# Kernel optimization log

Measured on AMD Instinct MI355X. Metric: run time of the kernel, lower is better.

The kernel has to match this reference:

```python
import jax, jax.numpy as jnp
import numpy as np

N_NODES = 50000
N_EDGES = 800000
D_IN = 128
D_OUT = 128


def _seg_mean(values, seg_ids, num_segments):
    # values: [E, D] gathered messages; seg_ids: [E] destination ids
    s = jax.ops.segment_sum(values, seg_ids, num_segments=num_segments)
    deg = jax.ops.segment_sum(jnp.ones((values.shape[0],), values.dtype), seg_ids,
                              num_segments=num_segments)
    # DGL mean aggregation yields 0 for zero in-degree nodes
    return jnp.where(deg[:, None] > 0, s / jnp.maximum(deg, 1.0)[:, None], 0.0)


def setup_inputs() -> dict:
    key = jax.random.key(0)
    k1, k2, k3, k4, k5 = jax.random.split(key, 5)
    feat = jax.random.normal(k1, (N_NODES, D_IN), dtype=jnp.float32)
    src = jax.random.randint(k2, (N_EDGES,), 0, N_NODES, dtype=jnp.int32)
    dst = jax.random.randint(k3, (N_EDGES,), 0, N_NODES, dtype=jnp.int32)
    W = jax.random.normal(k4, (D_OUT, 3 * D_IN), dtype=jnp.float32) * (1.0 / np.sqrt(3 * D_IN))
    b = jax.random.normal(k5, (D_OUT,), dtype=jnp.float32) * 0.01
    return {"feat": feat, "src": src, "dst": dst, "W": W, "b": b}


def reference(feat, src, dst, W, b):
    n = feat.shape[0]
    # forward direction: message from src -> dst, mean over in-neighbors
    fwd_neigh = _seg_mean(feat[src], dst, n)          # [N, D]
    # backward direction: graph.reverse() swaps src/dst
    bwd_neigh = _seg_mean(feat[dst], src, n)          # [N, D]
    h = jnp.concatenate((feat, fwd_neigh, bwd_neigh), axis=1)  # [N, 3D]
    return h @ W.T + b
```

## Files before the change

kernel.cpp:

```cpp
#include <hip/hip_runtime.h>

#define DIM 128
#define CAP 64
#define CHUNK 2048

typedef __attribute__((ext_vector_type(8))) short bf16x8;
typedef __attribute__((ext_vector_type(4))) float f32x4;
typedef __attribute__((ext_vector_type(2))) float f32x2;

__device__ __forceinline__ unsigned short f2b(float f) {
  unsigned int u = __float_as_uint(f);
  return (unsigned short)((u + 0x7FFFu + ((u >> 16) & 1u)) >> 16);
}
__device__ __forceinline__ float blo(unsigned int v) { return __uint_as_float(v << 16); }
__device__ __forceinline__ float bhi(unsigned int v) { return __uint_as_float(v & 0xFFFF0000u); }

__global__ __launch_bounds__(256) void k_bin(const int* __restrict__ src,
                                             const int* __restrict__ dst,
                                             unsigned int* __restrict__ scrF,
                                             unsigned int* __restrict__ scrB,
                                             int* __restrict__ offsF,
                                             int* __restrict__ offsB, int E) {
  __shared__ int fc[256], bc[256], fo[256], bo[256], sa[256], sb2[256];
  __shared__ unsigned int linf[CHUNK], linb[CHUNK];
  const int t = threadIdx.x;
  const int base = blockIdx.x * CHUNK;
  const int n = min(CHUNK, E - base);
  fc[t] = 0; bc[t] = 0;
  __syncthreads();
  int fbk[8], fsl[8], bsl[8], bbk[8];
  unsigned int fvv[8], bvv[8];
  #pragma unroll
  for (int j = 0; j < 8; ++j) {
    int e = base + j * 256 + t;
    fbk[j] = -1;
    if (e < E) {
      int s = src[e], d = dst[e];
      fbk[j] = d >> 8; fvv[j] = ((unsigned int)(d & 255) << 16) | (unsigned int)s;
      bbk[j] = s >> 8; bvv[j] = ((unsigned int)(s & 255) << 16) | (unsigned int)d;
      fsl[j] = atomicAdd(&fc[fbk[j]], 1);
      bsl[j] = atomicAdd(&bc[bbk[j]], 1);
    }
  }
  __syncthreads();
  sa[t] = fc[t]; sb2[t] = bc[t];
  __syncthreads();
  #pragma unroll
  for (int s = 1; s < 256; s <<= 1) {
    int va = sa[t] + ((t >= s) ? sa[t - s] : 0);
    int vb = sb2[t] + ((t >= s) ? sb2[t - s] : 0);
    __syncthreads();
    sa[t] = va; sb2[t] = vb;
    __syncthreads();
  }
  fo[t] = sa[t] - fc[t];
  bo[t] = sb2[t] - bc[t];
  __syncthreads();
  #pragma unroll
  for (int j = 0; j < 8; ++j) {
    if (fbk[j] >= 0) {
      linf[fo[fbk[j]] + fsl[j]] = fvv[j];
      linb[bo[bbk[j]] + bsl[j]] = bvv[j];
    }
  }
  offsF[blockIdx.x * 256 + t] = fo[t];
  offsB[blockIdx.x * 256 + t] = bo[t];
  __syncthreads();
  for (int k = t; k < n; k += 256) {
    scrF[base + k] = linf[k];
    scrB[base + k] = linb[k];
  }
}

__global__ __launch_bounds__(512) void k_gemmcsr(
    const float* __restrict__ feat, const float* __restrict__ W,
    const float* __restrict__ bias,
    unsigned short* __restrict__ g1b, unsigned char* __restrict__ g2f8,
    unsigned char* __restrict__ g3f8,
    const unsigned int* __restrict__ scrF, const unsigned int* __restrict__ scrB,
    const int* __restrict__ offsF, const int* __restrict__ offsB,
    unsigned short* __restrict__ fnbr, unsigned short* __restrict__ bnbr,
    int* __restrict__ degF, int* __restrict__ degB,
    int N, int E, int nblk, int nbkt, int G) {
  __shared__ __align__(16) unsigned char smem[98304];
  const int t = threadIdx.x;

  if ((int)blockIdx.x < 2 * nbkt) {
    int* ncnt = (int*)smem;
    unsigned short* nbuf = (unsigned short*)(smem + 1024);
    const int b = blockIdx.x >> 1;
    const int dir = blockIdx.x & 1;
    const unsigned int* scr = dir ? scrB : scrF;
    const int* offs = dir ? offsB : offsF;
    if (t < 256) ncnt[t] = 0;
    __syncthreads();
    for (int i = t; i < nblk; i += 512) {
      int o = offs[i * 256 + b];
      int n = min(CHUNK, E - i * CHUNK);
      int nxt = (b < 255) ? offs[i * 256 + b + 1] : n;
      int cb = i * CHUNK;
      for (int k = o; k < nxt; ++k) {
        unsigned int v = scr[cb + k];
        int node8 = v >> 16;
        int slot = atomicAdd(&ncnt[node8], 1);
        if (slot < CAP) nbuf[node8 * CAP + slot] = (unsigned short)(v & 0xFFFFu);
      }
    }
    __syncthreads();
    const int node0 = b * 256;
    const int nvalid = min(256, N - node0);
    if (nvalid <= 0) return;
    unsigned short* outp = (dir ? bnbr : fnbr) + (size_t)node0 * CAP;
    for (int idx = t; idx < nvalid * CAP; idx += 512)
      outp[idx] = nbuf[idx];
    int* deg = dir ? degB : degF;
    for (int u = t; u < nvalid; u += 512) deg[node0 + u] = ncnt[u];
    return;
  }

  for (int i = t; i < 12288; i += 512) {
    int flat = i * 4;
    int o = flat / 384;
    int kk = flat - o * 384;
    int n = (kk >> 7) * 128 + o;
    int k0 = kk & 127;
    float4 v = *(const float4*)(W + flat);
    ushort4 u; u.x = f2b(v.x); u.y = f2b(v.y); u.z = f2b(v.z); u.w = f2b(v.w);
    *(ushort4*)(smem + ((n * 256 + k0 * 2) ^ ((n & 7) << 4))) = u;
  }
  __syncthreads();

  const int wave = t >> 6, lane = t & 63;
  const int lr = lane & 15, lk = lane >> 4;
  float bv[8];
  #pragma unroll
  for (int i = 0; i < 8; ++i) bv[i] = bias[i * 16 + lr];

  const int MT = (N + 31) >> 5;
  const int TW = G * 8;
  for (int mt = (blockIdx.x - 2 * nbkt) * 8 + wave; mt < MT; mt += TW) {
    const int m0 = mt * 32;
    const bool two = (m0 + 16 < N);
    bf16x8 a0[4], a1[4];
    #pragma unroll
    for (int kc = 0; kc < 4; ++kc) {
      const float* p = feat + (size_t)(m0 + lr) * DIM + kc * 32 + lk * 8;
      float4 u = *(const float4*)p;
      float4 w = *(const float4*)(p + 4);
      bf16x8 r;
      r[0] = f2b(u.x); r[1] = f2b(u.y); r[2] = f2b(u.z); r[3] = f2b(u.w);
      r[4] = f2b(w.x); r[5] = f2b(w.y); r[6] = f2b(w.z); r[7] = f2b(w.w);
      a0[kc] = r;
    }
    if (two) {
      #pragma unroll
      for (int kc = 0; kc < 4; ++kc) {
        const float* p = feat + (size_t)(m0 + 16 + lr) * DIM + kc * 32 + lk * 8;
        float4 u = *(const float4*)p;
        float4 w = *(const float4*)(p + 4);
        bf16x8 r;
        r[0] = f2b(u.x); r[1] = f2b(u.y); r[2] = f2b(u.z); r[3] = f2b(u.w);
        r[4] = f2b(w.x); r[5] = f2b(w.y); r[6] = f2b(w.z); r[7] = f2b(w.w);
        a1[kc] = r;
      }
    }
    #pragma unroll
    for (int nf = 0; nf < 24; ++nf) {
      f32x4 acc0 = (f32x4){0.f, 0.f, 0.f, 0.f};
      f32x4 acc1 = (f32x4){0.f, 0.f, 0.f, 0.f};
      const int n = nf * 16 + lr;
      #pragma unroll
      for (int kc = 0; kc < 4; ++kc) {
        bf16x8 bw = *(const bf16x8*)(smem +
            ((n * 256 + kc * 64 + lk * 16) ^ ((n & 7) << 4)));
        acc0 = __builtin_amdgcn_mfma_f32_16x16x32_bf16(a0[kc], bw, acc0, 0, 0, 0);
        if (two)
          acc1 = __builtin_amdgcn_mfma_f32_16x16x32_bf16(a1[kc], bw, acc1, 0, 0, 0);
      }
      const int sec = nf >> 3;
      const int c0 = (nf & 7) * 16 + lr;
      if (sec == 0) {
        #pragma unroll
        for (int j = 0; j < 4; ++j) {
          g1b[(size_t)(m0 + lk * 4 + j) * DIM + c0] = f2b(acc0[j] + bv[nf & 7]);
          if (two)
            g1b[(size_t)(m0 + 16 + lk * 4 + j) * DIM + c0] = f2b(acc1[j] + bv[nf & 7]);
        }
      } else {
        unsigned char* gp = (sec == 1) ? g2f8 : g3f8;
        #pragma unroll
        for (int j = 0; j < 4; ++j) {
          unsigned int p8 = __builtin_amdgcn_cvt_pk_fp8_f32(acc0[j], acc0[j], 0, 0);
          gp[(size_t)(m0 + lk * 4 + j) * DIM + c0] = (unsigned char)p8;
          if (two) {
            unsigned int q8 = __builtin_amdgcn_cvt_pk_fp8_f32(acc1[j], acc1[j], 0, 0);
            gp[(size_t)(m0 + 16 + lk * 4 + j) * DIM + c0] = (unsigned char)q8;
          }
        }
      }
    }
  }
}

__global__ void k_aggregate(const unsigned char* __restrict__ g2f8,
                            const unsigned char* __restrict__ g3f8,
                            const unsigned short* __restrict__ g1b,
                            const int* __restrict__ degF, const int* __restrict__ degB,
                            const unsigned short* __restrict__ fnbr,
                            const unsigned short* __restrict__ bnbr,
                            float* __restrict__ out, int N) {
  int node = blockIdx.x * (blockDim.x >> 6) + (threadIdx.x >> 6);
  if (node >= N) return;
  const int lane = threadIdx.x & 63;
  const int qg = lane >> 4;
  const int sub = lane & 15;

  const int degf = degF[node], degb = degB[node];
  const int capf = min(degf, CAP), capb = min(degb, CAP);
  const int fid = fnbr[node * CAP + lane];
  const int bid = bnbr[node * CAP + lane];

  const uint2* gf = (const uint2*)g2f8;
  const uint2* gb = (const uint2*)g3f8;
  f32x2 f01 = {0.f, 0.f}, f23 = {0.f, 0.f}, f45 = {0.f, 0.f}, f67 = {0.f, 0.f};
  f32x2 b01 = {0.f, 0.f}, b23 = {0.f, 0.f}, b45 = {0.f, 0.f}, b67 = {0.f, 0.f};
  const int gmax = (max(capf, capb) + 3) >> 2;
  #pragma unroll 4
  for (int g = 0; g < gmax; ++g) {
    int k = 4 * g + qg;
    int rf = __shfl(fid, k);
    int rb = __shfl(bid, k);
    if (k < capf) {
      uint2 v = gf[rf * 16 + sub];
      f01 += __builtin_amdgcn_cvt_pk_f32_fp8(v.x, 0);
      f23 += __builtin_amdgcn_cvt_pk_f32_fp8(v.x, 1);
      f45 += __builtin_amdgcn_cvt_pk_f32_fp8(v.y, 0);
      f67 += __builtin_amdgcn_cvt_pk_f32_fp8(v.y, 1);
    }
    if (k < capb) {
      uint2 v = gb[rb * 16 + sub];
      b01 += __builtin_amdgcn_cvt_pk_f32_fp8(v.x, 0);
      b23 += __builtin_amdgcn_cvt_pk_f32_fp8(v.x, 1);
      b45 += __builtin_amdgcn_cvt_pk_f32_fp8(v.y, 0);
      b67 += __builtin_amdgcn_cvt_pk_f32_fp8(v.y, 1);
    }
  }
  float fa0 = f01[0], fa1 = f01[1], fa2 = f23[0], fa3 = f23[1];
  float fa4 = f45[0], fa5 = f45[1], fa6 = f67[0], fa7 = f67[1];
  float ba0 = b01[0], ba1 = b01[1], ba2 = b23[0], ba3 = b23[1];
  float ba4 = b45[0], ba5 = b45[1], ba6 = b67[0], ba7 = b67[1];
  fa0 += __shfl_xor(fa0, 16); fa0 += __shfl_xor(fa0, 32);
  fa1 += __shfl_xor(fa1, 16); fa1 += __shfl_xor(fa1, 32);
  fa2 += __shfl_xor(fa2, 16); fa2 += __shfl_xor(fa2, 32);
  fa3 += __shfl_xor(fa3, 16); fa3 += __shfl_xor(fa3, 32);
  fa4 += __shfl_xor(fa4, 16); fa4 += __shfl_xor(fa4, 32);
  fa5 += __shfl_xor(fa5, 16); fa5 += __shfl_xor(fa5, 32);
  fa6 += __shfl_xor(fa6, 16); fa6 += __shfl_xor(fa6, 32);
  fa7 += __shfl_xor(fa7, 16); fa7 += __shfl_xor(fa7, 32);
  ba0 += __shfl_xor(ba0, 16); ba0 += __shfl_xor(ba0, 32);
  ba1 += __shfl_xor(ba1, 16); ba1 += __shfl_xor(ba1, 32);
  ba2 += __shfl_xor(ba2, 16); ba2 += __shfl_xor(ba2, 32);
  ba3 += __shfl_xor(ba3, 16); ba3 += __shfl_xor(ba3, 32);
  ba4 += __shfl_xor(ba4, 16); ba4 += __shfl_xor(ba4, 32);
  ba5 += __shfl_xor(ba5, 16); ba5 += __shfl_xor(ba5, 32);
  ba6 += __shfl_xor(ba6, 16); ba6 += __shfl_xor(ba6, 32);
  ba7 += __shfl_xor(ba7, 16); ba7 += __shfl_xor(ba7, 32);

  if (lane < 16) {
    const float sf = (degf > 0) ? 1.0f / (float)degf : 0.0f;
    const float sb = (degb > 0) ? 1.0f / (float)degb : 0.0f;
    uint4 g1v = ((const uint4*)g1b)[node * 16 + lane];
    float4 u, v;
    u.x = blo(g1v.x) + fa0 * sf + ba0 * sb;
    u.y = bhi(g1v.x) + fa1 * sf + ba1 * sb;
    u.z = blo(g1v.y) + fa2 * sf + ba2 * sb;
    u.w = bhi(g1v.y) + fa3 * sf + ba3 * sb;
    v.x = blo(g1v.z) + fa4 * sf + ba4 * sb;
    v.y = bhi(g1v.z) + fa5 * sf + ba5 * sb;
    v.z = blo(g1v.w) + fa6 * sf + ba6 * sb;
    v.w = bhi(g1v.w) + fa7 * sf + ba7 * sb;
    float* op = out + node * DIM + lane * 8;
    *(float4*)op = u; *(float4*)(op + 4) = v;
  }
}

extern "C" void kernel_launch(void* const* d_in, const int* in_sizes, int n_in,
                              void* d_out, int out_size, void* d_ws, size_t ws_size,
                              hipStream_t stream) {
  (void)n_in; (void)out_size; (void)ws_size;
  const float* feat = (const float*)d_in[0];
  const int*   src  = (const int*)d_in[1];
  const int*   dst  = (const int*)d_in[2];
  const float* W    = (const float*)d_in[3];
  const float* bias = (const float*)d_in[4];
  float* out = (float*)d_out;
  const int N = in_sizes[0] / DIM;
  const int E = in_sizes[1];
  const int nblk = (E + CHUNK - 1) / CHUNK;
  const int nbkt = (N + 255) / 256;
  const int G = 192;

  char* ws = (char*)d_ws;
  size_t off = 0;
  auto take = [&](size_t bytes) -> void* {
    off = (off + 255) & ~(size_t)255;
    void* p = ws + off;
    off += bytes;
    return p;
  };
  unsigned int* scrF = (unsigned int*)take((size_t)nblk * CHUNK * 4);
  unsigned int* scrB = (unsigned int*)take((size_t)nblk * CHUNK * 4);
  int* offsF = (int*)take((size_t)nblk * 256 * 4);
  int* offsB = (int*)take((size_t)nblk * 256 * 4);
  unsigned short* fnbr = (unsigned short*)take((size_t)N * CAP * 2);
  unsigned short* bnbr = (unsigned short*)take((size_t)N * CAP * 2);
  int* degF = (int*)take((size_t)N * 4);
  int* degB = (int*)take((size_t)N * 4);
  unsigned short* g1b  = (unsigned short*)take((size_t)N * DIM * 2);
  unsigned char*  g2f8 = (unsigned char*)take((size_t)N * DIM);
  unsigned char*  g3f8 = (unsigned char*)take((size_t)N * DIM);

  k_bin<<<nblk, 256, 0, stream>>>(src, dst, scrF, scrB, offsF, offsB, E);
  k_gemmcsr<<<2 * nbkt + G, 512, 0, stream>>>(
      feat, W, bias, g1b, g2f8, g3f8, scrF, scrB, offsF, offsB,
      fnbr, bnbr, degF, degB, N, E, nblk, nbkt, G);
  k_aggregate<<<(N + 3) / 4, 256, 0, stream>>>(g2f8, g3f8, g1b, degF, degB,
                                               fnbr, bnbr, out, N);
}
```

Before: 99.53 us.

## Split GEMM output columns across block pairs and halve shared memory

The fused GEMM/CSR kernel now gives each GEMM block only half of the 384 output columns (192), with pairs of blocks sharing the same row tiles. This halves the bf16 weight tile in LDS to 48 KB, which may let more blocks co-reside per CU, and it moves GEMM blocks ahead of the CSR-bucketing blocks in launch order. The cost is that every feat row is loaded and converted twice, once per half, and the grid grows to 384 GEMM blocks. The CSR blocks share the same smaller LDS array; their 33 KB need still fits.

```diff
diff --git a/kernel.cpp b/kernel.cpp
--- a/kernel.cpp
+++ b/kernel.cpp
@@ -81,15 +81,16 @@
     const int* __restrict__ offsF, const int* __restrict__ offsB,
     unsigned short* __restrict__ fnbr, unsigned short* __restrict__ bnbr,
     int* __restrict__ degF, int* __restrict__ degB,
-    int N, int E, int nblk, int nbkt, int G) {
-  __shared__ __align__(16) unsigned char smem[98304];
+    int N, int E, int nblk, int nbkt, int NG) {
+  __shared__ __align__(16) unsigned char smem[49152];
   const int t = threadIdx.x;
 
-  if ((int)blockIdx.x < 2 * nbkt) {
+  if ((int)blockIdx.x >= NG) {
     int* ncnt = (int*)smem;
     unsigned short* nbuf = (unsigned short*)(smem + 1024);
-    const int b = blockIdx.x >> 1;
-    const int dir = blockIdx.x & 1;
+    const int cid = blockIdx.x - NG;
+    const int b = cid >> 1;
+    const int dir = cid & 1;
     const unsigned int* scr = dir ? scrB : scrF;
     const int* offs = dir ? offsB : offsF;
     if (t < 256) ncnt[t] = 0;
@@ -118,27 +119,30 @@
     return;
   }
 
-  for (int i = t; i < 12288; i += 512) {
-    int flat = i * 4;
-    int o = flat / 384;
-    int kk = flat - o * 384;
-    int n = (kk >> 7) * 128 + o;
-    int k0 = kk & 127;
-    float4 v = *(const float4*)(W + flat);
+  const int fl = blockIdx.x & 1;
+  for (int i = t; i < 6144; i += 512) {
+    int e = i * 4;
+    int nl = e >> 7;
+    int k0 = e & 127;
+    int n = fl * 192 + nl;
+    const float* wp = W + (size_t)(n & 127) * 384 + (n >> 7) * 128 + k0;
+    float4 v = *(const float4*)wp;
     ushort4 u; u.x = f2b(v.x); u.y = f2b(v.y); u.z = f2b(v.z); u.w = f2b(v.w);
-    *(ushort4*)(smem + ((n * 256 + k0 * 2) ^ ((n & 7) << 4))) = u;
+    *(ushort4*)(smem + ((nl * 256 + k0 * 2) ^ ((nl & 7) << 4))) = u;
   }
   __syncthreads();
 
   const int wave = t >> 6, lane = t & 63;
   const int lr = lane & 15, lk = lane >> 4;
   float bv[8];
-  #pragma unroll
-  for (int i = 0; i < 8; ++i) bv[i] = bias[i * 16 + lr];
+  if (fl == 0) {
+    #pragma unroll
+    for (int i = 0; i < 8; ++i) bv[i] = bias[i * 16 + lr];
+  }
 
   const int MT = (N + 31) >> 5;
-  const int TW = G * 8;
-  for (int mt = (blockIdx.x - 2 * nbkt) * 8 + wave; mt < MT; mt += TW) {
+  const int TW = (NG >> 1) * 8;
+  for (int mt = (blockIdx.x >> 1) * 8 + wave; mt < MT; mt += TW) {
     const int m0 = mt * 32;
     const bool two = (m0 + 16 < N);
     bf16x8 a0[4], a1[4];
@@ -165,20 +169,21 @@
       }
     }
     #pragma unroll
-    for (int nf = 0; nf < 24; ++nf) {
+    for (int nf = 0; nf < 12; ++nf) {
       f32x4 acc0 = (f32x4){0.f, 0.f, 0.f, 0.f};
       f32x4 acc1 = (f32x4){0.f, 0.f, 0.f, 0.f};
-      const int n = nf * 16 + lr;
+      const int nl = nf * 16 + lr;
       #pragma unroll
       for (int kc = 0; kc < 4; ++kc) {
         bf16x8 bw = *(const bf16x8*)(smem +
-            ((n * 256 + kc * 64 + lk * 16) ^ ((n & 7) << 4)));
+            ((nl * 256 + kc * 64 + lk * 16) ^ ((nl & 7) << 4)));
         acc0 = __builtin_amdgcn_mfma_f32_16x16x32_bf16(a0[kc], bw, acc0, 0, 0, 0);
         if (two)
           acc1 = __builtin_amdgcn_mfma_f32_16x16x32_bf16(a1[kc], bw, acc1, 0, 0, 0);
       }
-      const int sec = nf >> 3;
-      const int c0 = (nf & 7) * 16 + lr;
+      const int n = fl * 192 + nl;
+      const int sec = n >> 7;
+      const int c0 = n & 127;
       if (sec == 0) {
         #pragma unroll
         for (int j = 0; j < 4; ++j) {
@@ -298,7 +303,7 @@
   const int E = in_sizes[1];
   const int nblk = (E + CHUNK - 1) / CHUNK;
   const int nbkt = (N + 255) / 256;
-  const int G = 192;
+  const int NG = 384;
 
   char* ws = (char*)d_ws;
   size_t off = 0;
@@ -321,9 +326,9 @@
   unsigned char*  g3f8 = (unsigned char*)take((size_t)N * DIM);
 
   k_bin<<<nblk, 256, 0, stream>>>(src, dst, scrF, scrB, offsF, offsB, E);
-  k_gemmcsr<<<2 * nbkt + G, 512, 0, stream>>>(
+  k_gemmcsr<<<NG + 2 * nbkt, 512, 0, stream>>>(
       feat, W, bias, g1b, g2f8, g3f8, scrF, scrB, offsF, offsB,
-      fnbr, bnbr, degF, degB, N, E, nblk, nbkt, G);
+      fnbr, bnbr, degF, degB, N, E, nblk, nbkt, NG);
   k_aggregate<<<(N + 3) / 4, 256, 0, stream>>>(g2f8, g3f8, g1b, degF, degB,
                                                fnbr, bnbr, out, N);
 }
```

New measurement: 99.20 us. No clear change (-0.3%).
